# Kernel tuning notes

Measured on AMD Instinct MI355X. Metric: run time of the kernel, lower is better.

The kernel has to match this reference:

```python
import jax, jax.numpy as jnp
import numpy as np

L, H, E, D, FF, V, CTX = 8, 16, 1024, 64, 4096, 2048, 2048
B, T = 4, 1024


def _ln(x, g, b, eps=1e-5):
    mu = x.mean(-1, keepdims=True)
    var = ((x - mu) ** 2).mean(-1, keepdims=True)
    return (x - mu) * jax.lax.rsqrt(var + eps) * g + b


def setup_inputs() -> dict:
    key = jax.random.key(0)
    ks = jax.random.split(key, 12)
    s = 0.02
    return {
        "tokens": jax.random.randint(ks[0], (B, T), 0, V),
        "tok_emb": jax.random.normal(ks[1], (V, E), jnp.float32) * s,
        "pos_emb": jax.random.normal(ks[2], (CTX, E), jnp.float32) * s,
        "Wq": jax.random.normal(ks[3], (L, H, E, D), jnp.float32) * s,
        "Wk": jax.random.normal(ks[4], (L, H, E, D), jnp.float32) * s,
        "Wv": jax.random.normal(ks[5], (L, H, E, D), jnp.float32) * s,
        "Wo": jax.random.normal(ks[6], (L, H * D, E), jnp.float32) * s,
        "bo": jnp.zeros((L, E), jnp.float32),
        "ln1_g": jnp.ones((L, E), jnp.float32),
        "ln1_b": jnp.zeros((L, E), jnp.float32),
        "ln2_g": jnp.ones((L, E), jnp.float32),
        "ln2_b": jnp.zeros((L, E), jnp.float32),
        "W1": jax.random.normal(ks[7], (L, E, FF), jnp.float32) * s,
        "b1": jnp.zeros((L, FF), jnp.float32),
        "W2": jax.random.normal(ks[8], (L, FF, E), jnp.float32) * s,
        "b2": jnp.zeros((L, E), jnp.float32),
        "lnf_g": jnp.ones((E,), jnp.float32),
        "lnf_b": jnp.zeros((E,), jnp.float32),
        "Wlm": jax.random.normal(ks[9], (E, V), jnp.float32) * s,
        "blm": jnp.zeros((V,), jnp.float32),
    }


def reference(tokens, tok_emb, pos_emb, Wq, Wk, Wv, Wo, bo, ln1_g, ln1_b,
              ln2_g, ln2_b, W1, b1, W2, b2, lnf_g, lnf_b, Wlm, blm):
    # NOTE: original indexes pos_embd with token ids (pos_embd(x.int()))
    x = tok_emb[tokens] + pos_emb[tokens]  # [B,T,E]
    t = x.shape[1]
    causal = jnp.tril(jnp.ones((t, t), bool))
    scale = 1.0 / jnp.sqrt(jnp.float32(D))
    for l in range(L):
        x = _ln(x, ln1_g[l], ln1_b[l])
        q = jnp.einsum('bte,hed->bhtd', x, Wq[l])
        k = jnp.einsum('bte,hed->bhtd', x, Wk[l])
        v = jnp.einsum('bte,hed->bhtd', x, Wv[l])
        scores = jnp.einsum('bhtd,bhsd->bhts', q, k) * scale
        scores = jnp.where(causal, scores, -jnp.inf)
        att = jax.nn.softmax(scores, axis=-1)
        o = jnp.einsum('bhts,bhsd->bhtd', att, v)
        o = o.transpose(0, 2, 1, 3).reshape(x.shape[0], t, H * D)
        x = x + o @ Wo[l] + bo[l]
        x = _ln(x, ln2_g[l], ln2_b[l])
        x = x + jax.nn.relu(x @ W1[l] + b1[l]) @ W2[l] + b2[l]
    x = _ln(x, lnf_g, lnf_b)
    return x @ Wlm + blm
```

## Files before the change

### kernel.cpp

```cpp
#include <hip/hip_runtime.h>
#include <hip/hip_bf16.h>

#define LAYERS 8
#define H_ 16
#define E_ 1024
#define D_ 64
#define FF_ 4096
#define V_ 2048
#define B_ 4
#define T_ 1024
#define MTOK (B_*T_)

typedef __bf16 bf16x8_t __attribute__((ext_vector_type(8)));
typedef float f32x4_t __attribute__((ext_vector_type(4)));
typedef __hip_bfloat16 bf16_t;

__device__ __forceinline__ bf16_t f2b(float f) { return __float2bfloat16(f); }

__global__ void embed_kernel(const int* __restrict__ tokens,
                             const float* __restrict__ te,
                             const float* __restrict__ pe,
                             float* __restrict__ x) {
  int row = blockIdx.x;
  int tok = tokens[row];
  const float4* a = (const float4*)(te + (size_t)tok * E_);
  const float4* p = (const float4*)(pe + (size_t)tok * E_);
  float4* o = (float4*)(x + (size_t)row * E_);
  int t = threadIdx.x;
  float4 va = a[t], vp = p[t];
  o[t] = make_float4(va.x + vp.x, va.y + vp.y, va.z + vp.z, va.w + vp.w);
}

__global__ __launch_bounds__(256) void ln_kernel(float* __restrict__ x,
                                                 bf16_t* __restrict__ xb,
                                                 const float* __restrict__ g,
                                                 const float* __restrict__ b) {
  int row = blockIdx.x, tid = threadIdx.x;
  float* xr = x + (size_t)row * E_;
  float4 v = ((const float4*)xr)[tid];
  float s  = v.x + v.y + v.z + v.w;
  float sq = v.x*v.x + v.y*v.y + v.z*v.z + v.w*v.w;
  for (int off = 32; off; off >>= 1) {
    s  += __shfl_xor(s, off, 64);
    sq += __shfl_xor(sq, off, 64);
  }
  __shared__ float2 wred[4];
  if ((tid & 63) == 0) wred[tid >> 6] = make_float2(s, sq);
  __syncthreads();
  float2 w0 = wred[0], w1 = wred[1], w2 = wred[2], w3 = wred[3];
  float S = w0.x + w1.x + w2.x + w3.x, SQ = w0.y + w1.y + w2.y + w3.y;
  float mean = S * (1.0f / E_);
  float var  = SQ * (1.0f / E_) - mean * mean;
  float inv = rsqrtf(var + 1e-5f);
  float4 gv = ((const float4*)g)[tid];
  float4 bv = ((const float4*)b)[tid];
  float o0 = (v.x - mean) * inv * gv.x + bv.x;
  float o1 = (v.y - mean) * inv * gv.y + bv.y;
  float o2 = (v.z - mean) * inv * gv.z + bv.z;
  float o3 = (v.w - mean) * inv * gv.w + bv.w;
  ((float4*)xr)[tid] = make_float4(o0, o1, o2, o3);
  bf16_t* xo = xb + (size_t)row * E_ + tid * 4;
  xo[0] = f2b(o0); xo[1] = f2b(o1); xo[2] = f2b(o2); xo[3] = f2b(o3);
}

__global__ void transpose_kernel(const float* __restrict__ in, bf16_t* __restrict__ out,
                                 int R, int C) {
  __shared__ float tile[32][33];
  int z = blockIdx.z;
  const float* ib = in + (size_t)z * R * C;
  bf16_t* ob = out + (size_t)z * R * C;
  int r0 = blockIdx.y * 32, c0 = blockIdx.x * 32;
  int tx = threadIdx.x, ty = threadIdx.y;
  for (int i = 0; i < 4; i++)
    tile[ty + i * 8][tx] = ib[(size_t)(r0 + ty + i * 8) * C + (c0 + tx)];
  __syncthreads();
  for (int i = 0; i < 4; i++)
    ob[(size_t)(c0 + ty + i * 8) * R + (r0 + tx)] = f2b(tile[tx][ty + i * 8]);
}

#define BK 32

enum { MODE_F32 = 0, MODE_BF16 = 1, MODE_QKV = 2 };

__device__ __forceinline__ void gload16(const bf16_t* g, bf16_t* l) {
  __builtin_amdgcn_global_load_lds((const __attribute__((address_space(1))) void*)g,
                                   (__attribute__((address_space(3))) void*)l, 16, 0, 0);
}

__device__ __forceinline__ int xcd_swz(int flat, int nwg) {
  int q = nwg >> 3, r = nwg & 7;
  int xcd = flat & 7, idx = flat >> 3;
  return (xcd < r ? xcd * (q + 1) : r * (q + 1) + (xcd - r) * q) + idx;
}

template <int BM, int BN, int MODE>
__global__ __launch_bounds__(256) void gemm97_kernel(
    const bf16_t* __restrict__ A, long long sAz, int lda,
    const bf16_t* __restrict__ Bt, long long sBz, int ldb,
    void* __restrict__ C, long long sCz,
    const float* __restrict__ bias,
    const float* __restrict__ resid,
    int M, int N, int K, float alpha, int relu) {
  constexpr int FR = BM / 32, FC = BN / 32;
  constexpr int A_ISS = BM / 64, B_ISS = BN / 64;
  __shared__ __align__(16) bf16_t As[BM * BK];
  __shared__ __align__(16) bf16_t Bs[BN * BK];
  int tid = threadIdx.x;
  int z = blockIdx.z;
  int nwg = gridDim.x * gridDim.y;
  int flat = xcd_swz(blockIdx.y * gridDim.x + blockIdx.x, nwg);
  int m0 = (flat / gridDim.x) * BM, n0 = (flat % gridDim.x) * BN;
  const bf16_t* Ab = A + (size_t)z * sAz + (size_t)m0 * lda;
  const bf16_t* Bb = Bt + (size_t)z * sBz + (size_t)n0 * ldb;
  int lane = tid & 63, wave = tid >> 6;
  int wr = (wave >> 1) * (BM / 2), wc = (wave & 1) * (BN / 2);
  int lr = lane & 15, lk = (lane >> 4) * 8;
  int srow = tid >> 2;
  int scol = (tid & 3) * 8;

  f32x4_t acc[FR][FC];
  for (int i = 0; i < FR; i++)
    for (int j = 0; j < FC; j++)
      acc[i][j] = (f32x4_t){0.f, 0.f, 0.f, 0.f};

  for (int k0 = 0; k0 < K; k0 += BK) {
#pragma unroll
    for (int i = 0; i < A_ISS; i++)
      gload16(Ab + (size_t)(i * 64 + srow) * lda + k0 + scol, As + i * 2048 + wave * 512);
#pragma unroll
    for (int i = 0; i < B_ISS; i++)
      gload16(Bb + (size_t)(i * 64 + srow) * ldb + k0 + scol, Bs + i * 2048 + wave * 512);
    __syncthreads();
    bf16x8_t af[FR], bfv[FC];
#pragma unroll
    for (int i = 0; i < FR; i++)
      af[i] = *(const bf16x8_t*)(&As[(wr + i * 16 + lr) * BK + lk]);
#pragma unroll
    for (int j = 0; j < FC; j++)
      bfv[j] = *(const bf16x8_t*)(&Bs[(wc + j * 16 + lr) * BK + lk]);
#pragma unroll
    for (int i = 0; i < FR; i++)
#pragma unroll
      for (int j = 0; j < FC; j++)
        acc[i][j] = __builtin_amdgcn_mfma_f32_16x16x32_bf16(af[i], bfv[j], acc[i][j], 0, 0, 0);
    __syncthreads();
  }

#pragma unroll
  for (int i = 0; i < FR; i++)
#pragma unroll
    for (int j = 0; j < FC; j++) {
      f32x4_t v = acc[i][j];
      int n = n0 + wc + j * 16 + lr;
      int mb = m0 + wr + i * 16 + (lane >> 4) * 4;
#pragma unroll
      for (int r = 0; r < 4; r++) {
        int m = mb + r;
        float val = v[r] * alpha;
        if (bias) val += bias[n];
        if (relu) val = fmaxf(val, 0.f);
        if (MODE == MODE_F32) {
          size_t idx = (size_t)z * sCz + (size_t)m * N + n;
          ((float*)C)[idx] = val + (resid ? resid[idx] : 0.f);
        } else if (MODE == MODE_BF16) {
          size_t idx = (size_t)z * sCz + (size_t)m * N + n;
          ((bf16_t*)C)[idx] = f2b(val);
        } else {
          int sect = n >> 10, hd = n & 1023, h = hd >> 6, d = hd & 63;
          int b = m >> 10, t = m & 1023;
          size_t base = (size_t)sect * ((size_t)B_ * H_ * T_ * D_);
          size_t idx = base + ((size_t)(b * H_ + h) << 16) +
                       (sect == 2 ? (size_t)((d << 10) + t) : (size_t)((t << 6) + d));
          ((bf16_t*)C)[idx] = f2b(val);
        }
      }
    }
}

template <int NS>
__global__ __launch_bounds__(256) void splitk_reduce_kernel(const float* __restrict__ p,
                                                            float* __restrict__ x,
                                                            const float* __restrict__ bias) {
  size_t i = (size_t)blockIdx.x * 256 + threadIdx.x;
  float4 acc = ((float4*)x)[i];
  int n4 = (int)(i & (E_ / 4 - 1));
  float4 bv = ((const float4*)bias)[n4];
  acc.x += bv.x; acc.y += bv.y; acc.z += bv.z; acc.w += bv.w;
#pragma unroll
  for (int s = 0; s < NS; s++) {
    float4 a = ((const float4*)p)[i + (size_t)s * ((size_t)MTOK * E_ / 4)];
    acc.x += a.x; acc.y += a.y; acc.z += a.z; acc.w += a.w;
  }
  ((float4*)x)[i] = acc;
}

#define KPAD 72

__global__ __launch_bounds__(256) void flash_kernel(
    const bf16_t* __restrict__ q,
    const bf16_t* __restrict__ kk,
    const bf16_t* __restrict__ vt,
    bf16_t* __restrict__ o) {
  __shared__ __align__(16) bf16_t Ks[64 * KPAD];
  __shared__ __align__(16) bf16_t Vs[64 * KPAD];
  __shared__ __align__(16) bf16_t Ps[4][16 * KPAD];
  int bid = blockIdx.x;
  int qi = 15 - (bid >> 6);
  int bh = bid & 63;
  int b = bh >> 4, h = bh & 15;
  const bf16_t* qb = q + ((size_t)bh << 16);
  const bf16_t* kb = kk + ((size_t)bh << 16);
  const bf16_t* vb = vt + ((size_t)bh << 16);
  int tid = threadIdx.x, lane = tid & 63, wave = tid >> 6;
  int lr = lane & 15, lg = lane >> 4;
  int qbase = qi * 64;

  bf16x8_t qf[2];
  {
    const bf16_t* qrow = qb + (size_t)(qbase + wave * 16 + lr) * D_ + lg * 8;
    qf[0] = *(const bf16x8_t*)(qrow);
    qf[1] = *(const bf16x8_t*)(qrow + 32);
  }

  float m_r[4], l_r[4];
  f32x4_t oc[4];
#pragma unroll
  for (int r = 0; r < 4; r++) { m_r[r] = -1e30f; l_r[r] = 0.f; }
#pragma unroll
  for (int j = 0; j < 4; j++) oc[j] = (f32x4_t){0.f, 0.f, 0.f, 0.f};

  int srow = tid >> 2, scol = (tid & 3) * 16;

  for (int s = 0; s <= qi; s++) {
    int kv0 = s * 64;
    const bf16_t* kg = kb + (size_t)(kv0 + srow) * D_ + scol;
    bf16x8_t k0 = *(const bf16x8_t*)kg;
    bf16x8_t k1 = *(const bf16x8_t*)(kg + 8);
    const bf16_t* vg = vb + (size_t)srow * T_ + kv0 + scol;
    bf16x8_t v0 = *(const bf16x8_t*)vg;
    bf16x8_t v1 = *(const bf16x8_t*)(vg + 8);
    __syncthreads();
    *(bf16x8_t*)(&Ks[srow * KPAD + scol]) = k0;
    *(bf16x8_t*)(&Ks[srow * KPAD + scol + 8]) = k1;
    *(bf16x8_t*)(&Vs[srow * KPAD + scol]) = v0;
    *(bf16x8_t*)(&Vs[srow * KPAD + scol + 8]) = v1;
    __syncthreads();

    f32x4_t sc[4];
#pragma unroll
    for (int j = 0; j < 4; j++) {
      f32x4_t a = (f32x4_t){0.f, 0.f, 0.f, 0.f};
      bf16x8_t b0 = *(const bf16x8_t*)(&Ks[(j * 16 + lr) * KPAD + lg * 8]);
      bf16x8_t b1 = *(const bf16x8_t*)(&Ks[(j * 16 + lr) * KPAD + lg * 8 + 32]);
      a = __builtin_amdgcn_mfma_f32_16x16x32_bf16(qf[0], b0, a, 0, 0, 0);
      a = __builtin_amdgcn_mfma_f32_16x16x32_bf16(qf[1], b1, a, 0, 0, 0);
      sc[j] = a;
    }
    if (s == qi) {
#pragma unroll
      for (int j = 0; j < 4; j++)
#pragma unroll
        for (int r = 0; r < 4; r++) {
          int kvp = kv0 + j * 16 + lr;
          int qp  = qbase + wave * 16 + lg * 4 + r;
          sc[j][r] = (kvp <= qp) ? sc[j][r] * 0.125f : -1e30f;
        }
    } else {
#pragma unroll
      for (int j = 0; j < 4; j++)
#pragma unroll
        for (int r = 0; r < 4; r++) sc[j][r] *= 0.125f;
    }

    float ex[4];
#pragma unroll
    for (int r = 0; r < 4; r++) {
      float v = fmaxf(fmaxf(sc[0][r], sc[1][r]), fmaxf(sc[2][r], sc[3][r]));
      v = fmaxf(v, __shfl_xor(v, 1, 64));
      v = fmaxf(v, __shfl_xor(v, 2, 64));
      v = fmaxf(v, __shfl_xor(v, 4, 64));
      v = fmaxf(v, __shfl_xor(v, 8, 64));
      float mn = fmaxf(m_r[r], v);
      ex[r] = __expf(m_r[r] - mn);
      m_r[r] = mn;
      l_r[r] *= ex[r];
    }
#pragma unroll
    for (int j = 0; j < 4; j++)
#pragma unroll
      for (int r = 0; r < 4; r++) {
        float p = __expf(sc[j][r] - m_r[r]);
        l_r[r] += p;
        Ps[wave][(lg * 4 + r) * KPAD + j * 16 + lr] = f2b(p);
      }

#pragma unroll
    for (int j = 0; j < 4; j++)
#pragma unroll
      for (int r = 0; r < 4; r++) oc[j][r] *= ex[r];

    bf16x8_t pa0 = *(const bf16x8_t*)(&Ps[wave][lr * KPAD + lg * 8]);
    bf16x8_t pa1 = *(const bf16x8_t*)(&Ps[wave][lr * KPAD + lg * 8 + 32]);
#pragma unroll
    for (int j = 0; j < 4; j++) {
      bf16x8_t vb0 = *(const bf16x8_t*)(&Vs[(j * 16 + lr) * KPAD + lg * 8]);
      bf16x8_t vb1 = *(const bf16x8_t*)(&Vs[(j * 16 + lr) * KPAD + lg * 8 + 32]);
      oc[j] = __builtin_amdgcn_mfma_f32_16x16x32_bf16(pa0, vb0, oc[j], 0, 0, 0);
      oc[j] = __builtin_amdgcn_mfma_f32_16x16x32_bf16(pa1, vb1, oc[j], 0, 0, 0);
    }
  }

#pragma unroll
  for (int r = 0; r < 4; r++) {
    float v = l_r[r];
    v += __shfl_xor(v, 1, 64);
    v += __shfl_xor(v, 2, 64);
    v += __shfl_xor(v, 4, 64);
    v += __shfl_xor(v, 8, 64);
    l_r[r] = 1.f / v;
  }
  bf16_t* ob = o + ((size_t)(b * T_ + qbase + wave * 16)) * (H_ * D_) + h * D_;
#pragma unroll
  for (int j = 0; j < 4; j++)
#pragma unroll
    for (int r = 0; r < 4; r++) {
      int qrow = lg * 4 + r;
      ob[(size_t)qrow * (H_ * D_) + j * 16 + lr] = f2b(oc[j][r] * l_r[r]);
    }
}

extern "C" void kernel_launch(void* const* d_in, const int* in_sizes, int n_in,
                              void* d_out, int out_size, void* d_ws, size_t ws_size,
                              hipStream_t stream) {
  (void)in_sizes; (void)n_in; (void)out_size;
  const int*   tokens = (const int*)d_in[0];
  const float* tok_emb = (const float*)d_in[1];
  const float* pos_emb = (const float*)d_in[2];
  const float* Wq = (const float*)d_in[3];
  const float* Wk = (const float*)d_in[4];
  const float* Wv = (const float*)d_in[5];
  const float* Wo = (const float*)d_in[6];
  const float* bo = (const float*)d_in[7];
  const float* ln1_g = (const float*)d_in[8];
  const float* ln1_b = (const float*)d_in[9];
  const float* ln2_g = (const float*)d_in[10];
  const float* ln2_b = (const float*)d_in[11];
  const float* W1 = (const float*)d_in[12];
  const float* b1 = (const float*)d_in[13];
  const float* W2 = (const float*)d_in[14];
  const float* b2 = (const float*)d_in[15];
  const float* lnf_g = (const float*)d_in[16];
  const float* lnf_b = (const float*)d_in[17];
  const float* Wlm = (const float*)d_in[18];
  const float* blm = (const float*)d_in[19];

  char* w = (char*)d_ws;
  size_t off = 0;
  auto alloc = [&](size_t bytes) { void* p = (void*)(w + off); off += (bytes + 255) & ~(size_t)255; return p; };
  float*  x    = (float*)alloc((size_t)MTOK * E_ * 4);
  bf16_t* xb   = (bf16_t*)alloc((size_t)MTOK * E_ * 2);
  bf16_t* q    = (bf16_t*)alloc((size_t)B_ * H_ * T_ * D_ * 2);
  bf16_t* kk   = (bf16_t*)alloc((size_t)B_ * H_ * T_ * D_ * 2);
  bf16_t* vt   = (bf16_t*)alloc((size_t)B_ * H_ * T_ * D_ * 2);
  bf16_t* o    = (bf16_t*)alloc((size_t)MTOK * E_ * 2);
  bf16_t* h1   = (bf16_t*)alloc((size_t)MTOK * FF_ * 2);
  bf16_t* WqkvT = (bf16_t*)alloc((size_t)3 * E_ * H_ * D_ * 2);
  bf16_t* WoT  = (bf16_t*)alloc((size_t)E_ * H_ * D_ * 2);
  bf16_t* W1T  = (bf16_t*)alloc((size_t)E_ * FF_ * 2);
  bf16_t* W2T  = (bf16_t*)alloc((size_t)E_ * FF_ * 2);
  bf16_t* WlmT = (bf16_t*)alloc((size_t)E_ * V_ * 2);
  size_t pk_bytes = (size_t)4 * MTOK * E_ * 4;
  bool do_splitk = (ws_size > off + pk_bytes + (1 << 20));
  float* p4 = do_splitk ? (float*)alloc(pk_bytes) : nullptr;

  embed_kernel<<<MTOK, 256, 0, stream>>>(tokens, tok_emb, pos_emb, x);
  transpose_kernel<<<dim3(V_ / 32, E_ / 32, 1), dim3(32, 8), 0, stream>>>(Wlm, WlmT, E_, V_);

  for (int l = 0; l < LAYERS; l++) {
    ln_kernel<<<MTOK, 256, 0, stream>>>(x, xb, ln1_g + l * E_, ln1_b + l * E_);

    transpose_kernel<<<dim3(D_ / 32, E_ / 32, H_), dim3(32, 8), 0, stream>>>(
        Wq + (size_t)l * H_ * E_ * D_, WqkvT, E_, D_);
    transpose_kernel<<<dim3(D_ / 32, E_ / 32, H_), dim3(32, 8), 0, stream>>>(
        Wk + (size_t)l * H_ * E_ * D_, WqkvT + (size_t)E_ * H_ * D_, E_, D_);
    transpose_kernel<<<dim3(D_ / 32, E_ / 32, H_), dim3(32, 8), 0, stream>>>(
        Wv + (size_t)l * H_ * E_ * D_, WqkvT + (size_t)2 * E_ * H_ * D_, E_, D_);
    transpose_kernel<<<dim3(E_ / 32, (H_ * D_) / 32, 1), dim3(32, 8), 0, stream>>>(
        Wo + (size_t)l * H_ * D_ * E_, WoT, H_ * D_, E_);
    transpose_kernel<<<dim3(FF_ / 32, E_ / 32, 1), dim3(32, 8), 0, stream>>>(
        W1 + (size_t)l * E_ * FF_, W1T, E_, FF_);
    transpose_kernel<<<dim3(E_ / 32, FF_ / 32, 1), dim3(32, 8), 0, stream>>>(
        W2 + (size_t)l * FF_ * E_, W2T, FF_, E_);

    gemm97_kernel<128, 128, MODE_QKV><<<dim3(24, 32, 1), 256, 0, stream>>>(
        xb, 0, E_, WqkvT, 0, E_, q, 0, nullptr, nullptr, MTOK, 3 * H_ * D_, E_, 1.f, 0);

    flash_kernel<<<1024, 256, 0, stream>>>(q, kk, vt, o);

    if (do_splitk) {
      gemm97_kernel<128, 128, MODE_F32><<<dim3(8, 32, 2), 256, 0, stream>>>(
          o, 512, H_ * D_, WoT, 512, H_ * D_, p4, (long long)MTOK * E_,
          nullptr, nullptr, MTOK, E_, (H_ * D_) / 2, 1.f, 0);
      splitk_reduce_kernel<2><<<MTOK * E_ / 1024, 256, 0, stream>>>(p4, x, bo + l * E_);
    } else {
      gemm97_kernel<128, 128, MODE_F32><<<dim3(8, 32, 1), 256, 0, stream>>>(
          o, 0, H_ * D_, WoT, 0, H_ * D_, x, 0, bo + l * E_, x, MTOK, E_, H_ * D_, 1.f, 0);
    }

    ln_kernel<<<MTOK, 256, 0, stream>>>(x, xb, ln2_g + l * E_, ln2_b + l * E_);

    gemm97_kernel<128, 128, MODE_BF16><<<dim3(32, 32, 1), 256, 0, stream>>>(
        xb, 0, E_, W1T, 0, E_, h1, 0, b1 + l * FF_, nullptr, MTOK, FF_, E_, 1.f, 1);
    if (do_splitk) {
      gemm97_kernel<128, 128, MODE_F32><<<dim3(8, 32, 4), 256, 0, stream>>>(
          h1, 1024, FF_, W2T, 1024, FF_, p4, (long long)MTOK * E_,
          nullptr, nullptr, MTOK, E_, FF_ / 4, 1.f, 0);
      splitk_reduce_kernel<4><<<MTOK * E_ / 1024, 256, 0, stream>>>(p4, x, b2 + l * E_);
    } else {
      gemm97_kernel<128, 128, MODE_F32><<<dim3(8, 32, 1), 256, 0, stream>>>(
          h1, 0, FF_, W2T, 0, FF_, x, 0, b2 + l * E_, x, MTOK, E_, FF_, 1.f, 0);
    }
  }

  ln_kernel<<<MTOK, 256, 0, stream>>>(x, xb, lnf_g, lnf_b);
  gemm97_kernel<128, 128, MODE_F32><<<dim3(16, 32, 1), 256, 0, stream>>>(
      xb, 0, E_, WlmT, 0, E_, d_out, 0, blm, nullptr, MTOK, V_, E_, 1.f, 0);
}
```

Measured before the change: 2.547 ms.

## Double-buffer GEMM LDS tiles and prefetch next K/V block in attention

The GEMM kernel now keeps two LDS buffers and issues the global-to-LDS loads for the next K tile before computing on the current one. This removes one barrier per iteration and overlaps memory latency with MFMA work. The attention kernel prefetches the next K/V block into registers while computing the current block, hiding the global load latency. In exchange, GEMM LDS use doubles, which may lower occupancy, and the attention kernel holds more live registers. The GEMM relies on the async gload16 completing before the single barrier at the end of each iteration.

New measurement: 2.391 ms. 1.06x faster.

```diff
diff --git a/kernel.cpp b/kernel.cpp
--- a/kernel.cpp
+++ b/kernel.cpp
@@ -103,8 +103,8 @@
     int M, int N, int K, float alpha, int relu) {
   constexpr int FR = BM / 32, FC = BN / 32;
   constexpr int A_ISS = BM / 64, B_ISS = BN / 64;
-  __shared__ __align__(16) bf16_t As[BM * BK];
-  __shared__ __align__(16) bf16_t Bs[BN * BK];
+  __shared__ __align__(16) bf16_t As[2][BM * BK];
+  __shared__ __align__(16) bf16_t Bs[2][BN * BK];
   int tid = threadIdx.x;
   int z = blockIdx.z;
   int nwg = gridDim.x * gridDim.y;
@@ -123,27 +123,35 @@
     for (int j = 0; j < FC; j++)
       acc[i][j] = (f32x4_t){0.f, 0.f, 0.f, 0.f};
 
-  for (int k0 = 0; k0 < K; k0 += BK) {
+  auto stage = [&](int buf, int k0) {
 #pragma unroll
     for (int i = 0; i < A_ISS; i++)
-      gload16(Ab + (size_t)(i * 64 + srow) * lda + k0 + scol, As + i * 2048 + wave * 512);
+      gload16(Ab + (size_t)(i * 64 + srow) * lda + k0 + scol, &As[buf][i * 2048 + wave * 512]);
 #pragma unroll
     for (int i = 0; i < B_ISS; i++)
-      gload16(Bb + (size_t)(i * 64 + srow) * ldb + k0 + scol, Bs + i * 2048 + wave * 512);
-    __syncthreads();
+      gload16(Bb + (size_t)(i * 64 + srow) * ldb + k0 + scol, &Bs[buf][i * 2048 + wave * 512]);
+  };
+
+  int nk = K / BK;
+  stage(0, 0);
+  __syncthreads();
+  int cur = 0;
+  for (int kt = 0; kt < nk; ++kt) {
+    if (kt + 1 < nk) stage(cur ^ 1, (kt + 1) * BK);
     bf16x8_t af[FR], bfv[FC];
 #pragma unroll
     for (int i = 0; i < FR; i++)
-      af[i] = *(const bf16x8_t*)(&As[(wr + i * 16 + lr) * BK + lk]);
+      af[i] = *(const bf16x8_t*)(&As[cur][(wr + i * 16 + lr) * BK + lk]);
 #pragma unroll
     for (int j = 0; j < FC; j++)
-      bfv[j] = *(const bf16x8_t*)(&Bs[(wc + j * 16 + lr) * BK + lk]);
+      bfv[j] = *(const bf16x8_t*)(&Bs[cur][(wc + j * 16 + lr) * BK + lk]);
 #pragma unroll
     for (int i = 0; i < FR; i++)
 #pragma unroll
       for (int j = 0; j < FC; j++)
         acc[i][j] = __builtin_amdgcn_mfma_f32_16x16x32_bf16(af[i], bfv[j], acc[i][j], 0, 0, 0);
     __syncthreads();
+    cur ^= 1;
   }
 
 #pragma unroll
@@ -231,14 +239,17 @@
 
   int srow = tid >> 2, scol = (tid & 3) * 16;
 
+  bf16x8_t k0, k1, v0, v1;
+  {
+    const bf16_t* kg = kb + (size_t)srow * D_ + scol;
+    k0 = *(const bf16x8_t*)kg;
+    k1 = *(const bf16x8_t*)(kg + 8);
+    const bf16_t* vg = vb + (size_t)srow * T_ + scol;
+    v0 = *(const bf16x8_t*)vg;
+    v1 = *(const bf16x8_t*)(vg + 8);
+  }
+
   for (int s = 0; s <= qi; s++) {
-    int kv0 = s * 64;
-    const bf16_t* kg = kb + (size_t)(kv0 + srow) * D_ + scol;
-    bf16x8_t k0 = *(const bf16x8_t*)kg;
-    bf16x8_t k1 = *(const bf16x8_t*)(kg + 8);
-    const bf16_t* vg = vb + (size_t)srow * T_ + kv0 + scol;
-    bf16x8_t v0 = *(const bf16x8_t*)vg;
-    bf16x8_t v1 = *(const bf16x8_t*)(vg + 8);
     __syncthreads();
     *(bf16x8_t*)(&Ks[srow * KPAD + scol]) = k0;
     *(bf16x8_t*)(&Ks[srow * KPAD + scol + 8]) = k1;
@@ -246,6 +257,17 @@
     *(bf16x8_t*)(&Vs[srow * KPAD + scol + 8]) = v1;
     __syncthreads();
 
+    if (s < qi) {
+      int kv1 = (s + 1) * 64;
+      const bf16_t* kg = kb + (size_t)(kv1 + srow) * D_ + scol;
+      k0 = *(const bf16x8_t*)kg;
+      k1 = *(const bf16x8_t*)(kg + 8);
+      const bf16_t* vg = vb + (size_t)srow * T_ + kv1 + scol;
+      v0 = *(const bf16x8_t*)vg;
+      v1 = *(const bf16x8_t*)(vg + 8);
+    }
+
+    int kv0 = s * 64;
     f32x4_t sc[4];
 #pragma unroll
     for (int j = 0; j < 4; j++) {
```
